# Kernel optimization log

Hardware: AMD Instinct MI355X
Metric: run time of the kernel (lower is better)

## Reference

```python
import jax, jax.numpy as jnp
import numpy as np
import math

L_LAYERS = 2; B = 2; SEQ = 1024; D = 512; N = 16; H = 8; DH = 64; P = 32; KC = 4; DTR = 32

def _silu(x):
    return x * jax.nn.sigmoid(x)

def _rms(x, w, eps=1e-6):
    return x * jax.lax.rsqrt(jnp.mean(x * x, axis=-1, keepdims=True) + eps) * w

def _mamba(x, Win, conv_w, conv_b, Wx, Wdt, bdt, Alog, Dp, Wout):
    # x: [b,l,d]; mamba-ssm reference math with expand=1 (d_inner == d)
    b, l, d = x.shape
    xz = x @ Win                                   # [b,l,2d]
    xc, z = jnp.split(xz, 2, axis=-1)
    xp = jnp.pad(xc, ((0, 0), (KC - 1, 0), (0, 0)))  # causal depthwise conv
    xc = sum(xp[:, k:k + l, :] * conv_w[:, k] for k in range(KC)) + conv_b
    xc = _silu(xc)
    dbl = xc @ Wx                                  # [b,l,dtr+2N]
    dt = dbl[..., :DTR]
    Bc = dbl[..., DTR:DTR + N]                     # [b,l,N]
    Cc = dbl[..., DTR + N:]                        # [b,l,N]
    dt = jax.nn.softplus(dt @ Wdt + bdt)           # [b,l,d]
    A = -jnp.exp(Alog)                             # [d,N]
    dA = jnp.exp(dt[..., None] * A)                # [b,l,d,N]
    dBu = dt[..., None] * Bc[:, :, None, :] * xc[..., None]  # [b,l,d,N]
    def step(h, inp):
        dA_t, dBu_t, C_t = inp
        h = dA_t * h + dBu_t                       # [b,d,N]
        return h, jnp.einsum('bdn,bn->bd', h, C_t)
    h0 = jnp.zeros((b, d, N), x.dtype)
    _, ys = jax.lax.scan(step, h0, (dA.transpose(1, 0, 2, 3), dBu.transpose(1, 0, 2, 3), Cc.transpose(1, 0, 2)))
    y = ys.transpose(1, 0, 2) + Dp * xc
    y = y * _silu(z)
    return y @ Wout

def _enformer_attn(q, k, vv, u, vb, w):
    # q,k,vv: [b,l,h,d]; u,vb: [h,d]; w: [h,d,P]
    b, l, h, d = q.shape
    Pd = w.shape[-1]
    pos = jnp.arange(l)
    dist = pos[None, :] - pos[:, None]             # [l,l]
    pow_rate = jnp.exp(jnp.log((l + 1) / 2.0) / (Pd // 2))
    cw = pow_rate ** jnp.arange(1, Pd // 2 + 1, dtype=jnp.float32)
    ub = (jnp.abs(dist)[:, :, None].astype(jnp.float32) <= cw)
    sb = jnp.sign(dist)[:, :, None].astype(jnp.float32) * ub.astype(jnp.float32)
    basis = jnp.concatenate([ub.astype(jnp.float32), sb], axis=-1)  # [l,l,P]
    scale = 1.0 / math.sqrt(d)
    # qr_term without materializing r[h,l,l,d]: (q@w) then contract with basis
    qw = jnp.einsum('bihd,hdn->bhin', q, w)
    qr = jnp.einsum('bhin,ijn->bhij', qw, basis)
    uk = jnp.einsum('hd,bjhd->bhj', u, k)[:, :, None, :]
    vr = jnp.einsum('hn,ijn->hij', jnp.einsum('hd,hdn->hn', vb, w), basis)
    scores = jnp.einsum('bihd,bjhd->bhij', q, k) * scale + (qr + uk + vr[None]) * scale
    attn = jax.nn.softmax(scores, axis=-1)
    return jnp.einsum('bhij,bjhd->bihd', attn, vv)

def _forward(x, rms_m, W_in, b_in, m_Win, m_conv_w, m_conv_b, m_Wx, m_Wdt, m_bdt, m_Alog, m_D, m_Wout, W_out, b_out, rms_a, Wq, Wk, Wv, u, v, w_rel, Wo, b_o):
    b, l, dm = x.shape
    for i in range(L_LAYERS):
        # --- BidirectionalMamba block (tie_in_proj=True, tie_gate=False) ---
        skip = x
        xn = _rms(x, rms_m[i])
        proj = xn @ W_in[i] + b_in[i]              # [b,l,3*dm]
        xf = proj[..., :dm]
        zf = proj[..., dm:2 * dm]
        zr = proj[..., 2 * dm:]
        yf = _mamba(xf, m_Win[i, 0], m_conv_w[i, 0], m_conv_b[i, 0], m_Wx[i, 0], m_Wdt[i, 0], m_bdt[i, 0], m_Alog[i, 0], m_D[i, 0], m_Wout[i, 0])
        yr = jnp.flip(_mamba(jnp.flip(xf, axis=1), m_Win[i, 1], m_conv_w[i, 1], m_conv_b[i, 1], m_Wx[i, 1], m_Wdt[i, 1], m_bdt[i, 1], m_Alog[i, 1], m_D[i, 1], m_Wout[i, 1]), axis=1)
        y = yf * _silu(zf) + yr * _silu(zr)
        x = y @ W_out[i] + b_out[i] + skip
        # --- Enformer relative-position attention block ---
        skip = x
        xn = _rms(x, rms_a[i])
        q = (xn @ Wq[i]).reshape(b, l, H, DH)
        k = (xn @ Wk[i]).reshape(b, l, H, DH)
        vv = (xn @ Wv[i]).reshape(b, l, H, DH)
        o = _enformer_attn(q, k, vv, u[i], v[i], w_rel[i]).reshape(b, l, H * DH)
        x = skip + o @ Wo[i] + b_o[i]
    return x

def setup_inputs() -> dict:
    key = jax.random.key(0)
    ks = iter(jax.random.split(key, 48))
    def rn(shape, s=0.02):
        return jax.random.normal(next(ks), shape, dtype=jnp.float32) * s
    L = L_LAYERS
    inp = {}
    inp['x'] = jax.random.normal(next(ks), (B, SEQ, D), dtype=jnp.float32)
    inp['rms_m'] = jnp.ones((L, D), jnp.float32)
    inp['W_in'] = rn((L, D, 3 * D)); inp['b_in'] = jnp.zeros((L, 3 * D), jnp.float32)
    inp['m_Win'] = rn((L, 2, D, 2 * D))
    inp['m_conv_w'] = rn((L, 2, D, KC), 0.1); inp['m_conv_b'] = jnp.zeros((L, 2, D), jnp.float32)
    inp['m_Wx'] = rn((L, 2, D, DTR + 2 * N))
    inp['m_Wdt'] = rn((L, 2, DTR, D), 0.1); inp['m_bdt'] = rn((L, 2, D), 0.5)
    inp['m_Alog'] = jnp.tile(jnp.log(jnp.arange(1, N + 1, dtype=jnp.float32)), (L, 2, D, 1))
    inp['m_D'] = jnp.ones((L, 2, D), jnp.float32)
    inp['m_Wout'] = rn((L, 2, D, D))
    inp['W_out'] = rn((L, D, D)); inp['b_out'] = jnp.zeros((L, D), jnp.float32)
    inp['rms_a'] = jnp.ones((L, D), jnp.float32)
    inp['Wq'] = rn((L, D, H * DH)); inp['Wk'] = rn((L, D, H * DH)); inp['Wv'] = rn((L, D, H * DH))
    inp['u'] = rn((L, H, DH), 0.1); inp['v'] = rn((L, H, DH), 0.1)
    inp['w_rel'] = rn((L, H, DH, P), 0.1)
    inp['Wo'] = rn((L, H * DH, D)); inp['b_o'] = jnp.zeros((L, D), jnp.float32)
    return inp

def reference(x, rms_m, W_in, b_in, m_Win, m_conv_w, m_conv_b, m_Wx, m_Wdt, m_bdt, m_Alog, m_D, m_Wout, W_out, b_out, rms_a, Wq, Wk, Wv, u, v, w_rel, Wo, b_o):
    return _forward(x, rms_m, W_in, b_in, m_Win, m_conv_w, m_conv_b, m_Wx, m_Wdt, m_bdt, m_Alog, m_D, m_Wout, W_out, b_out, rms_a, Wq, Wk, Wv, u, v, w_rel, Wo, b_o)
```

## Files before the change

kernel.cpp:

```cpp
#include <hip/hip_runtime.h>

#define LL 2
#define BB 2
#define SEQL 1024
#define DD 512
#define NN 16
#define HH 8
#define DHH 64
#define PPB 32
#define KCC 4
#define DTRR 32

#define GBS 4
#define TC 64
#define NC (SEQL / TC)
#define NR (GBS * DD * NN)

#define AR_L     4325376L
#define OFF_WIN  0L
#define OFF_MWIN 786432L
#define OFF_WT2  1835008L
#define OFF_MWOUT 2490368L
#define OFF_WOUT 3014656L
#define OFF_QKV  3276800L
#define OFF_WO   4063232L

typedef __attribute__((ext_vector_type(8))) short bf16x8;
typedef __attribute__((ext_vector_type(4))) short short4v;
typedef __attribute__((ext_vector_type(4))) float f32x4;

__device__ __forceinline__ float siluf(float x) { return x / (1.f + expf(-x)); }
__device__ __forceinline__ float softplusf(float x) { return x > 20.f ? x : log1pf(expf(x)); }

__device__ __forceinline__ unsigned short f2bf(float x) {
  union { float f; unsigned u; } v; v.f = x;
  unsigned r = v.u + 0x7fff + ((v.u >> 16) & 1);
  return (unsigned short)(r >> 16);
}

__device__ __forceinline__ bf16x8 ld_frag(const unsigned short* p) {
  short4v a = *(const short4v*)(p);
  short4v b = *(const short4v*)(p + 4);
  bf16x8 r;
  r[0]=a[0]; r[1]=a[1]; r[2]=a[2]; r[3]=a[3];
  r[4]=b[0]; r[5]=b[1]; r[6]=b[2]; r[7]=b[3];
  return r;
}

__device__ __forceinline__ bf16x8 pack8(const float* p) {
  bf16x8 r;
  #pragma unroll
  for (int e = 0; e < 8; e++) r[e] = (short)f2bf(p[e]);
  return r;
}

struct TD { const float* src; unsigned short* dst; int ldsrc; int K; int N; int t0; };
struct TDs { TD a[24]; };

__global__ __launch_bounds__(256) void wtrans_all(TDs ds)
{
  int bid = blockIdx.x;
  int mi = 0;
  #pragma unroll 1
  for (int i = 1; i < 24; i++) if (bid >= ds.a[i].t0) mi = i;
  TD d = ds.a[mi];
  int local = bid - d.t0;
  int tilesN = d.N >> 5;
  int tn = local % tilesN, tk = local / tilesN;
  __shared__ float t[32][33];
  int tx = threadIdx.x & 31, ty = threadIdx.x >> 5;
  int n0 = tn * 32, k0 = tk * 32;
  #pragma unroll
  for (int i = 0; i < 4; i++)
    t[ty + 8 * i][tx] = d.src[(long)(k0 + ty + 8 * i) * d.ldsrc + n0 + tx];
  __syncthreads();
  #pragma unroll
  for (int i = 0; i < 4; i++)
    d.dst[(long)(n0 + ty + 8 * i) * d.K + k0 + tx] = f2bf(t[tx][ty + 8 * i]);
}

__global__ __launch_bounds__(256) void weff_kernel(
    const float* __restrict__ Wx, const float* __restrict__ Wdt,
    unsigned short* __restrict__ WTA)
{
  int lg = blockIdx.z;
  int l = lg >> 1, g = lg & 1;
  const float* wx = Wx + (long)(l * 2 + g) * DD * 64;
  const float* wd = Wdt + (long)(l * 2 + g) * DTRR * DD;
  unsigned short* wt = WTA + (long)l * AR_L + OFF_WT2 + (long)g * 327680;
  int n0 = blockIdx.x * 32, k0 = blockIdx.y * 32;
  __shared__ float wx_s[32][33];
  __shared__ float wd_s[32][33];
  int tx = threadIdx.x & 31, ty = threadIdx.x >> 5;
  #pragma unroll
  for (int i = 0; i < 4; i++) {
    wx_s[ty + 8 * i][tx] = wx[(long)(k0 + ty + 8 * i) * 64 + tx];
    wd_s[ty + 8 * i][tx] = wd[(long)(ty + 8 * i) * DD + n0 + tx];
  }
  __syncthreads();
  #pragma unroll
  for (int i = 0; i < 4; i++) {
    int nl = ty + 8 * i;
    float s = 0.f;
    #pragma unroll
    for (int r = 0; r < 32; r++) s = fmaf(wx_s[tx][r], wd_s[r][nl], s);
    wt[(long)(n0 + nl) * DD + k0 + tx] = f2bf(s);
  }
}

__global__ __launch_bounds__(256) void rmsinv_kernel(
    const float* __restrict__ x, float* __restrict__ inv)
{
  int row = blockIdx.x * 4 + (threadIdx.x >> 6);
  int lane = threadIdx.x & 63;
  const float* xr = x + (long)row * DD;
  float4 a = *(const float4*)(xr + lane * 4);
  float4 b = *(const float4*)(xr + 256 + lane * 4);
  float s = a.x*a.x + a.y*a.y + a.z*a.z + a.w*a.w + b.x*b.x + b.y*b.y + b.z*b.z + b.w*b.w;
  for (int o = 32; o; o >>= 1) s += __shfl_down(s, o);
  if (lane == 0) inv[row] = rsqrtf(s / (float)DD + 1e-6f);
}

template<int BM, int BN>
__global__ __launch_bounds__(256) void gemm_bf16_t(
    const float* __restrict__ A, const unsigned short* __restrict__ WT,
    const float* __restrict__ bias, const float* __restrict__ resid,
    const float* __restrict__ invrow, const float* __restrict__ colw,
    float* __restrict__ C,
    int M, int N, int K, int lda, int ldc,
    long aBatch, long wBatch, long biasBatch, long cBatch,
    int aflipL, int act)
{
  constexpr int FM = BM / 32;
  constexpr int FN = BN / 32;
  int g = blockIdx.z;
  A  += (long)g * aBatch;
  WT += (long)g * wBatch;
  C  += (long)g * cBatch;
  if (bias) bias += (long)g * biasBatch;
  const bool flip = (aflipL > 0) && (g == 1);

  __shared__ unsigned short A_lds[BM][72];
  __shared__ unsigned short B_lds[BN][72];
  int tid = threadIdx.x;
  int w = tid >> 6, lane = tid & 63, li = lane & 15, lg = lane >> 4;
  int bm = blockIdx.y * BM, bn = blockIdx.x * BN;
  int wm = (w & 1) * (BM / 2), wn = (w >> 1) * (BN / 2);
  f32x4 acc[FM][FN] = {};

  const int kqA = (tid & 15) * 4, r0A = tid >> 4;
  const int kqB = (tid & 7) * 8,  r0B = tid >> 3;

  for (int k0 = 0; k0 < K; k0 += 64) {
    __syncthreads();
    float4 cw4 = {1.f, 1.f, 1.f, 1.f};
    if (colw) cw4 = *(const float4*)(colw + k0 + kqA);
    #pragma unroll
    for (int i = 0; i < BM / 16; i++) {
      int m = bm + r0A + 16 * i;
      int mm = m;
      if (flip) { int bb = m / aflipL; int t = m - bb * aflipL; mm = bb * aflipL + (aflipL - 1 - t); }
      float4 av = *(const float4*)(A + (long)mm * lda + k0 + kqA);
      float sc = invrow ? invrow[mm] : 1.f;
      short4v ap = { (short)f2bf(av.x * sc * cw4.x), (short)f2bf(av.y * sc * cw4.y),
                     (short)f2bf(av.z * sc * cw4.z), (short)f2bf(av.w * sc * cw4.w) };
      *(short4v*)(&A_lds[r0A + 16 * i][kqA]) = ap;
    }
    #pragma unroll
    for (int i = 0; i < BN / 32; i++) {
      int n = bn + r0B + 32 * i;
      bf16x8 bv = *(const bf16x8*)(WT + (long)n * K + k0 + kqB);
      *(bf16x8*)(&B_lds[r0B + 32 * i][kqB]) = bv;
    }
    __syncthreads();
    #pragma unroll
    for (int ks = 0; ks < 2; ks++) {
      bf16x8 af[FM], bfr[FN];
      #pragma unroll
      for (int fm = 0; fm < FM; fm++)
        af[fm] = *(const bf16x8*)(&A_lds[wm + fm * 16 + li][ks * 32 + lg * 8]);
      #pragma unroll
      for (int fn = 0; fn < FN; fn++)
        bfr[fn] = *(const bf16x8*)(&B_lds[wn + fn * 16 + li][ks * 32 + lg * 8]);
      #pragma unroll
      for (int fm = 0; fm < FM; fm++)
        #pragma unroll
        for (int fn = 0; fn < FN; fn++)
          acc[fm][fn] = __builtin_amdgcn_mfma_f32_16x16x32_bf16(af[fm], bfr[fn], acc[fm][fn], 0, 0, 0);
    }
  }
  #pragma unroll
  for (int fm = 0; fm < FM; fm++) {
    #pragma unroll
    for (int fn = 0; fn < FN; fn++) {
      int n = bn + wn + fn * 16 + li;
      float bv = bias ? bias[n] : 0.f;
      #pragma unroll
      for (int r = 0; r < 4; r++) {
        int m = bm + wm + fm * 16 + 4 * lg + r;
        float v = acc[fm][fn][r] + bv;
        if (act == 1) v = softplusf(v);
        if (resid) v += resid[(long)m * ldc + n];
        C[(long)m * ldc + n] = v;
      }
    }
  }
}

__global__ __launch_bounds__(256) void gemm_dtbc(
    const float* __restrict__ A, const unsigned short* __restrict__ WT2,
    const float* __restrict__ bdt, float* __restrict__ dtv, float* __restrict__ bc,
    int layer)
{
  int g = blockIdx.z;
  A   += (long)g * BB * SEQL * DD;
  WT2 += (long)g * 640 * DD;
  dtv += (long)g * BB * SEQL * DD;
  bc  += (long)g * BB * SEQL * 32;
  bdt += (long)(layer * 2 + g) * DD;

  __shared__ unsigned short A_lds[64][72];
  __shared__ unsigned short B_lds[64][72];
  int tid = threadIdx.x;
  int w = tid >> 6, lane = tid & 63, li = lane & 15, lg = lane >> 4;
  int bm = blockIdx.y * 64, bn = blockIdx.x * 64;
  int wm = (w & 1) * 32, wn = (w >> 1) * 32;
  f32x4 acc[2][2] = {};

  const int kqA = (tid & 15) * 4, r0A = tid >> 4;
  const int kqB = (tid & 7) * 8,  r0B = tid >> 3;

  for (int k0 = 0; k0 < DD; k0 += 64) {
    __syncthreads();
    #pragma unroll
    for (int i = 0; i < 4; i++) {
      int m = bm + r0A + 16 * i;
      float4 av = *(const float4*)(A + (long)m * DD + k0 + kqA);
      short4v ap = { (short)f2bf(av.x), (short)f2bf(av.y), (short)f2bf(av.z), (short)f2bf(av.w) };
      *(short4v*)(&A_lds[r0A + 16 * i][kqA]) = ap;
    }
    #pragma unroll
    for (int i = 0; i < 2; i++) {
      int n = bn + r0B + 32 * i;
      bf16x8 bv = *(const bf16x8*)(WT2 + (long)n * DD + k0 + kqB);
      *(bf16x8*)(&B_lds[r0B + 32 * i][kqB]) = bv;
    }
    __syncthreads();
    #pragma unroll
    for (int ks = 0; ks < 2; ks++) {
      bf16x8 af[2], bfr[2];
      #pragma unroll
      for (int fm = 0; fm < 2; fm++)
        af[fm] = *(const bf16x8*)(&A_lds[wm + fm * 16 + li][ks * 32 + lg * 8]);
      #pragma unroll
      for (int fn = 0; fn < 2; fn++)
        bfr[fn] = *(const bf16x8*)(&B_lds[wn + fn * 16 + li][ks * 32 + lg * 8]);
      #pragma unroll
      for (int fm = 0; fm < 2; fm++)
        #pragma unroll
        for (int fn = 0; fn < 2; fn++)
          acc[fm][fn] = __builtin_amdgcn_mfma_f32_16x16x32_bf16(af[fm], bfr[fn], acc[fm][fn], 0, 0, 0);
    }
  }
  #pragma unroll
  for (int fm = 0; fm < 2; fm++) {
    #pragma unroll
    for (int fn = 0; fn < 2; fn++) {
      int n = bn + wn + fn * 16 + li;
      if (n < 512) {
        float bv = bdt[n];
        #pragma unroll
        for (int r = 0; r < 4; r++) {
          int m = bm + wm + fm * 16 + 4 * lg + r;
          dtv[(long)m * DD + n] = softplusf(acc[fm][fn][r] + bv);
        }
      } else if (n < 544) {
        #pragma unroll
        for (int r = 0; r < 4; r++) {
          int m = bm + wm + fm * 16 + 4 * lg + r;
          bc[(long)m * 32 + (n - 512)] = acc[fm][fn][r];
        }
      }
    }
  }
}

__global__ __launch_bounds__(256) void conv_silu_kernel(
    const float* __restrict__ xz, const float* __restrict__ cw, const float* __restrict__ cb,
    float* __restrict__ xc, int layer)
{
  long idx = (long)blockIdx.x * 256 + threadIdx.x;
  int c = idx % DD;
  long r = idx / DD;
  int t = r % SEQL;
  long gb = r / SEQL;
  int g = (int)(gb / BB);
  const float* w = cw + ((long)(layer * 2 + g) * DD + c) * KCC;
  float acc = cb[(long)(layer * 2 + g) * DD + c];
  const float* xp = xz + (r - t) * 2 * DD + c;
  #pragma unroll
  for (int k = 0; k < KCC; k++) {
    int tt = t - (KCC - 1) + k;
    if (tt >= 0) acc = fmaf(xp[(long)tt * 2 * DD], w[k], acc);
  }
  xc[idx] = siluf(acc);
}

__global__ __launch_bounds__(256) void scan_chunk_kernel(
    const float* __restrict__ dtv, const float* __restrict__ xc,
    const float* __restrict__ bc, const float* __restrict__ Alog,
    float* __restrict__ P, float* __restrict__ Hend, int layer)
{
  int chunk = blockIdx.x, dtile = blockIdx.y, gb = blockIdx.z;
  int g = gb / BB;
  int tid = threadIdx.x;
  int n = tid & 15, dl = tid >> 4;
  int d = dtile * 16 + dl;
  int t0 = chunk * TC;
  __shared__ float dtv_s[TC][16], xc_s[TC][16], B_s[TC][17];
  {
    int c = tid & 15, rr = tid >> 4;
    long base = ((long)gb * SEQL + t0) * DD + dtile * 16;
    long dbase = ((long)gb * SEQL + t0) * 32;
    #pragma unroll
    for (int i = 0; i < 4; i++) {
      int tl = rr + i * 16;
      dtv_s[tl][c] = dtv[base + (long)tl * DD + c];
      xc_s[tl][c]  = xc[base + (long)tl * DD + c];
      B_s[tl][c]   = bc[dbase + (long)tl * 32 + c];
    }
  }
  __syncthreads();
  float a = -expf(Alog[((long)((layer * 2 + g) * DD) + d) * NN + n]);
  float h = 0.f, sdt = 0.f;
  #pragma unroll 4
  for (int t = 0; t < TC; t++) {
    float dt = dtv_s[t][dl];
    float dA = expf(dt * a);
    h = fmaf(dA, h, dt * B_s[t][n] * xc_s[t][dl]);
    sdt += dt;
  }
  int r = (gb * DD + d) * NN + n;
  long o = (long)chunk * NR + r;
  P[o] = expf(a * sdt);
  Hend[o] = h;
}

__global__ __launch_bounds__(256) void scan_combine_kernel(
    const float* __restrict__ P, const float* __restrict__ Hend, float* __restrict__ Hin)
{
  int r = blockIdx.x * 256 + threadIdx.x;
  float h = 0.f;
  #pragma unroll
  for (int c = 0; c < NC; c++) {
    Hin[(long)c * NR + r] = h;
    h = fmaf(P[(long)c * NR + r], h, Hend[(long)c * NR + r]);
  }
}

__global__ __launch_bounds__(256) void scan_apply_kernel(
    const float* __restrict__ dtv, const float* __restrict__ xc, const float* __restrict__ xz,
    const float* __restrict__ bc, const float* __restrict__ Alog, const float* __restrict__ Dp,
    const float* __restrict__ Hin, float* __restrict__ ym, int layer)
{
  int chunk = blockIdx.x, dtile = blockIdx.y, gb = blockIdx.z;
  int g = gb / BB;
  int tid = threadIdx.x;
  int n = tid & 15, dl = tid >> 4;
  int d = dtile * 16 + dl;
  int t0 = chunk * TC;
  __shared__ float dtv_s[TC][16], xc_s[TC][16], B_s[TC][17], C_s[TC][17], y_s[TC][16];
  {
    int c = tid & 15, rr = tid >> 4;
    long base = ((long)gb * SEQL + t0) * DD + dtile * 16;
    long dbase = ((long)gb * SEQL + t0) * 32;
    #pragma unroll
    for (int i = 0; i < 4; i++) {
      int tl = rr + i * 16;
      dtv_s[tl][c] = dtv[base + (long)tl * DD + c];
      xc_s[tl][c]  = xc[base + (long)tl * DD + c];
      B_s[tl][c]   = bc[dbase + (long)tl * 32 + c];
      C_s[tl][c]   = bc[dbase + (long)tl * 32 + 16 + c];
    }
  }
  __syncthreads();
  float a = -expf(Alog[((long)((layer * 2 + g) * DD) + d) * NN + n]);
  int r = (gb * DD + d) * NN + n;
  float h = Hin[(long)chunk * NR + r];
  #pragma unroll 4
  for (int t = 0; t < TC; t++) {
    float dt = dtv_s[t][dl];
    float dA = expf(dt * a);
    h = fmaf(dA, h, dt * B_s[t][n] * xc_s[t][dl]);
    float val = h * C_s[t][n];
    val += __shfl_xor(val, 1);
    val += __shfl_xor(val, 2);
    val += __shfl_xor(val, 4);
    val += __shfl_xor(val, 8);
    if (n == 0) y_s[t][dl] = val;
  }
  __syncthreads();
  {
    int c = tid & 15, rr = tid >> 4;
    long base = ((long)gb * SEQL + t0) * DD + dtile * 16;
    long zbase = ((long)gb * SEQL + t0) * 2 * DD + DD + dtile * 16;
    float Dpc = Dp[(long)(layer * 2 + g) * DD + dtile * 16 + c];
    #pragma unroll
    for (int i = 0; i < 4; i++) {
      int tl = rr + i * 16;
      float z = xz[zbase + (long)tl * 2 * DD + c];
      ym[base + (long)tl * DD + c] = (y_s[tl][c] + Dpc * xc_s[tl][c]) * siluf(z);
    }
  }
}

__global__ __launch_bounds__(256) void combine_kernel(
    const float* __restrict__ yp, const float* __restrict__ proj, float* __restrict__ yc)
{
  long idx = (long)blockIdx.x * 256 + threadIdx.x;
  int d = idx % DD;
  long r = idx / DD;
  int t = r % SEQL;
  long b = r / SEQL;
  float y0 = yp[idx];
  float y1 = yp[(long)BB * SEQL * DD + (b * SEQL + (SEQL - 1 - t)) * (long)DD + d];
  const float* pr = proj + r * 3 * DD;
  float zf = pr[DD + d];
  float zr = pr[2 * DD + d];
  yc[idx] = y0 * siluf(zf) + y1 * siluf(zr);
}

__global__ void tab_kernel(unsigned short* __restrict__ tab)
{
  int idx = blockIdx.x * blockDim.x + threadIdx.x;
  if (idx >= 2047) return;
  int di = idx - 1023;
  int ad = di < 0 ? -di : di;
  float pr = expf(logf((SEQL + 1) * 0.5f) / 16.0f);
  int n0 = 16;
  for (int n = 15; n >= 0; n--) {
    float cw = powf(pr, (float)(n + 1));
    if ((float)ad <= cw) n0 = n;
  }
  tab[idx] = (unsigned short)(di == 0 ? 34 : (di < 0 ? n0 : 17 + n0));
}

__global__ __launch_bounds__(256) void qw_kernel(
    const float* __restrict__ q, const float* __restrict__ w_rel, float* __restrict__ S, int layer)
{
  int itile = blockIdx.x;
  int bh = blockIdx.y;
  int h = bh % HH, b = bh / HH;
  int i0 = itile * 64;
  __shared__ float q_s[64][65];
  __shared__ float w_s[64][33];
  __shared__ float qwn[64][33];
  int tid = threadIdx.x;
  {
    int r = tid >> 2, c4 = (tid & 3) * 16;
    const float* qr = q + ((long)(b * SEQL + i0 + r)) * DD + h * 64 + c4;
    #pragma unroll
    for (int e = 0; e < 4; e++) {
      float4 v = *(const float4*)(qr + e * 4);
      q_s[r][c4 + e * 4 + 0] = v.x; q_s[r][c4 + e * 4 + 1] = v.y;
      q_s[r][c4 + e * 4 + 2] = v.z; q_s[r][c4 + e * 4 + 3] = v.w;
    }
  }
  for (int idx = tid; idx < 64 * 32; idx += 256) {
    int d = idx >> 5, n = idx & 31;
    w_s[d][n] = w_rel[((long)(layer * HH + h) * DHH + d) * PPB + n];
  }
  __syncthreads();
  {
    int i = tid & 63, ngrp = tid >> 6;
    float acc[8] = {};
    #pragma unroll 8
    for (int d = 0; d < 64; d++) {
      float qv = q_s[i][d];
      #pragma unroll
      for (int e = 0; e < 8; e++) acc[e] = fmaf(qv, w_s[d][ngrp * 8 + e], acc[e]);
    }
    #pragma unroll
    for (int e = 0; e < 8; e++) qwn[i][ngrp * 8 + e] = acc[e];
  }
  __syncthreads();
  for (int idx = tid; idx < 64 * 17; idx += 256) {
    int il = idx / 17, m = idx % 17;
    float s1 = 0.f, s2 = 0.f;
    for (int n = m; n < 16; n++) { s1 += qwn[il][n]; s2 += qwn[il][16 + n]; }
    float* Sp = S + ((long)bh * SEQL + i0 + il) * 34;
    Sp[m] = s1;
    Sp[17 + m] = s2;
  }
}

__global__ __launch_bounds__(256) void vw_kernel(
    const float* __restrict__ vparam, const float* __restrict__ w_rel, float* __restrict__ VS, int layer)
{
  __shared__ float vws[HH][PPB];
  int tid = threadIdx.x;
  int h = tid / PPB, n = tid % PPB;
  const float* vp = vparam + (long)(layer * HH + h) * DHH;
  const float* wp = w_rel + ((long)(layer * HH + h) * DHH) * PPB + n;
  float s = 0.f;
  for (int d = 0; d < DHH; d++) s = fmaf(vp[d], wp[d * PPB], s);
  vws[h][n] = s;
  __syncthreads();
  if (tid < HH * 17) {
    int hh = tid / 17, m = tid % 17;
    float s1 = 0.f, s2 = 0.f;
    for (int nn = m; nn < 16; nn++) { s1 += vws[hh][nn]; s2 += vws[hh][16 + nn]; }
    VS[hh * 34 + m] = s1;
    VS[hh * 34 + 17 + m] = s2;
  }
}

__global__ __launch_bounds__(256) void uk_kernel(
    const float* __restrict__ u, const float* __restrict__ k, float* __restrict__ uk, int layer)
{
  int wid = (blockIdx.x * 256 + threadIdx.x) >> 6;
  int lane = threadIdx.x & 63;
  if (wid >= BB * HH * SEQL) return;
  int j = wid % SEQL;
  int bh = wid / SEQL;
  int h = bh % HH;
  int b = bh / HH;
  float vv = u[(long)(layer * HH + h) * DHH + lane] * k[((long)(b * SEQL + j) * HH + h) * DHH + lane];
  for (int o = 32; o; o >>= 1) vv += __shfl_down(vv, o);
  if (lane == 0) uk[(long)bh * SEQL + j] = vv;
}

__global__ __launch_bounds__(256) void attn_mfma_kernel(
    const float* __restrict__ q, const float* __restrict__ k, const float* __restrict__ vv,
    const float* __restrict__ S, const float* __restrict__ VS, const float* __restrict__ uk,
    const unsigned short* __restrict__ tab, float* __restrict__ out)
{
  __shared__ __align__(16) char smem[39680];
  unsigned short* K_lds  = (unsigned short*)(smem);
  unsigned short* VT_lds = (unsigned short*)(smem + 8704);
  unsigned short* PT_lds = (unsigned short*)(smem + 17408);
  float* E               = (float*)(smem + 26112);
  unsigned short* tab_s  = (unsigned short*)(smem + 35328);
  float* uk_s            = (float*)(smem + 39424);
  float* O_lds           = (float*)(smem);

  int itile = blockIdx.x;
  int bh = blockIdx.y;
  int h = bh % HH, b = bh / HH;
  int i0 = itile * 64;
  int tid = threadIdx.x;
  int w = tid >> 6;
  int lane = tid & 63;
  int li = lane & 15, lg = lane >> 4;

  for (int idx = tid; idx < 64 * 17; idx += 256) {
    int il = idx / 17, m = idx % 17;
    long srow = ((long)bh * SEQL + i0 + il) * 34;
    float c0 = S[srow + m]      + VS[h * 34 + m];
    float c1 = S[srow + 17 + m] + VS[h * 34 + 17 + m];
    E[il * 36 + m]      = c0 - c1;
    E[il * 36 + 17 + m] = c0 + c1;
    if (m == 0) E[il * 36 + 34] = c0;
  }
  for (int idx = tid; idx < 2047; idx += 256) tab_s[idx] = tab[idx];

  int iq = i0 + w * 16 + li;
  const float* qrow = q + ((long)(b * SEQL + iq)) * DD + h * 64;
  bf16x8 qf0 = pack8(qrow + 8 * lg);
  bf16x8 qf1 = pack8(qrow + 32 + 8 * lg);

  f32x4 oacc[4] = {};
  float mrun = -1e30f, lrun = 0.f;
  const int ibase = i0 + w * 16 + li;
  unsigned short* PTw = PT_lds + w * 16 * 68;
  const float* Erow = E + (w * 16 + li) * 36;

  for (int j0 = 0; j0 < SEQL; j0 += 64) {
    __syncthreads();
    {
      int jl = tid >> 4;
      int dq = (tid & 15) * 4;
      #pragma unroll
      for (int rr = 0; rr < 4; rr++) {
        int jj = jl + rr * 16;
        long grow = ((long)(b * SEQL + j0 + jj)) * DD + h * 64 + dq;
        float4 kv = *(const float4*)(k + grow);
        short4v kp = { (short)f2bf(kv.x), (short)f2bf(kv.y), (short)f2bf(kv.z), (short)f2bf(kv.w) };
        *(short4v*)(K_lds + jj * 68 + dq) = kp;
        float4 vvv = *(const float4*)(vv + grow);
        VT_lds[(dq + 0) * 68 + jj] = f2bf(vvv.x);
        VT_lds[(dq + 1) * 68 + jj] = f2bf(vvv.y);
        VT_lds[(dq + 2) * 68 + jj] = f2bf(vvv.z);
        VT_lds[(dq + 3) * 68 + jj] = f2bf(vvv.w);
      }
      if (tid < 64) uk_s[tid] = uk[(long)bh * SEQL + j0 + tid];
    }
    __syncthreads();

    f32x4 sf[4];
    #pragma unroll
    for (int jj = 0; jj < 4; jj++) {
      f32x4 c = {};
      c = __builtin_amdgcn_mfma_f32_16x16x32_bf16(
            ld_frag(K_lds + (jj * 16 + li) * 68 + 8 * lg), qf0, c, 0, 0, 0);
      c = __builtin_amdgcn_mfma_f32_16x16x32_bf16(
            ld_frag(K_lds + (jj * 16 + li) * 68 + 32 + 8 * lg), qf1, c, 0, 0, 0);
      sf[jj] = c;
    }

    float sv[4][4];
    float tmax = -1e30f;
    #pragma unroll
    for (int jj = 0; jj < 4; jj++) {
      #pragma unroll
      for (int r = 0; r < 4; r++) {
        int jloc = jj * 16 + 4 * lg + r;
        int di = (j0 + jloc) - ibase;
        int id = tab_s[1023 + di];
        float val = (sf[jj][r] + Erow[id] + uk_s[jloc]) * 0.125f;
        sv[jj][r] = val;
        tmax = fmaxf(tmax, val);
      }
    }
    tmax = fmaxf(tmax, __shfl_xor(tmax, 16));
    tmax = fmaxf(tmax, __shfl_xor(tmax, 32));
    float mnew = fmaxf(mrun, tmax);
    float fsc = __expf(mrun - mnew);
    mrun = mnew;
    lrun *= fsc;
    #pragma unroll
    for (int df = 0; df < 4; df++) oacc[df] *= fsc;

    float psum = 0.f;
    #pragma unroll
    for (int jj = 0; jj < 4; jj++) {
      short4v pk;
      #pragma unroll
      for (int r = 0; r < 4; r++) {
        float p = __expf(sv[jj][r] - mnew);
        psum += p;
        pk[r] = (short)f2bf(p);
      }
      *(short4v*)(PTw + li * 68 + jj * 16 + 4 * lg) = pk;
    }
    psum += __shfl_xor(psum, 16);
    psum += __shfl_xor(psum, 32);
    lrun += psum;

    asm volatile("s_waitcnt lgkmcnt(0)" ::: "memory");

    bf16x8 pf0 = ld_frag(PTw + li * 68 + 8 * lg);
    bf16x8 pf1 = ld_frag(PTw + li * 68 + 32 + 8 * lg);
    #pragma unroll
    for (int df = 0; df < 4; df++) {
      f32x4 c = oacc[df];
      c = __builtin_amdgcn_mfma_f32_16x16x32_bf16(
            ld_frag(VT_lds + (df * 16 + li) * 68 + 8 * lg), pf0, c, 0, 0, 0);
      c = __builtin_amdgcn_mfma_f32_16x16x32_bf16(
            ld_frag(VT_lds + (df * 16 + li) * 68 + 32 + 8 * lg), pf1, c, 0, 0, 0);
      oacc[df] = c;
    }
  }

  __syncthreads();
  float inv = 1.f / lrun;
  #pragma unroll
  for (int df = 0; df < 4; df++) {
    f32x4 o = oacc[df] * inv;
    *(f32x4*)(O_lds + (w * 16 + li) * 68 + df * 16 + 4 * lg) = o;
  }
  __syncthreads();
  {
    int il = tid >> 2, c0 = (tid & 3) * 16;
    long orow = ((long)(b * SEQL + i0 + il)) * DD + h * 64 + c0;
    #pragma unroll
    for (int c4 = 0; c4 < 4; c4++) {
      f32x4 o = *(const f32x4*)(O_lds + il * 68 + c0 + c4 * 4);
      *(f32x4*)(out + orow + c4 * 4) = o;
    }
  }
}

extern "C" void kernel_launch(void* const* d_in, const int* in_sizes, int n_in,
                              void* d_out, int out_size, void* d_ws, size_t ws_size,
                              hipStream_t stream) {
  const float* x_in     = (const float*)d_in[0];
  const float* rms_m    = (const float*)d_in[1];
  const float* W_in     = (const float*)d_in[2];
  const float* b_in     = (const float*)d_in[3];
  const float* m_Win    = (const float*)d_in[4];
  const float* m_conv_w = (const float*)d_in[5];
  const float* m_conv_b = (const float*)d_in[6];
  const float* m_Wx     = (const float*)d_in[7];
  const float* m_Wdt    = (const float*)d_in[8];
  const float* m_bdt    = (const float*)d_in[9];
  const float* m_Alog   = (const float*)d_in[10];
  const float* m_Dp     = (const float*)d_in[11];
  const float* m_Wout   = (const float*)d_in[12];
  const float* W_out    = (const float*)d_in[13];
  const float* b_out    = (const float*)d_in[14];
  const float* rms_a    = (const float*)d_in[15];
  const float* Wq       = (const float*)d_in[16];
  const float* Wk       = (const float*)d_in[17];
  const float* Wv       = (const float*)d_in[18];
  const float* u_p      = (const float*)d_in[19];
  const float* v_p      = (const float*)d_in[20];
  const float* w_rel    = (const float*)d_in[21];
  const float* Wo       = (const float*)d_in[22];
  const float* b_o      = (const float*)d_in[23];
  float* out = (float*)d_out;

  float* ws = (float*)d_ws;
  const long U = (long)BB * SEQL * DD;
  float* xA    = ws;
  float* xB    = ws + 1 * U;
  float* xn    = ws + 2 * U;
  float* proj  = ws + 3 * U;
  float* xz    = ws + 6 * U;
  float* xc    = ws + 10 * U;
  float* dtv   = ws + 12 * U;
  float* ym    = ws + 14 * U;
  float* ycomb = ws + 16 * U;
  float* smallb= ws + 17 * U;
  float* bcbuf = smallb;
  float* ukbuf = smallb + 262144;
  float* Sbuf  = smallb + 278528;
  float* VSbuf = smallb + 835584;
  unsigned short* tabg = (unsigned short*)(smallb + 835856);
  float* invm  = smallb + 836880;
  float* inva  = smallb + 838928;
  unsigned short* WTA = (unsigned short*)(ws + 18 * U);
  float* yp = xz;
  float* qb = proj;
  float* kb = proj + U;
  float* vb = proj + 2 * U;
  float* attnout = ym;
  float* Pbuf = xn;
  float* Hend = xn + (long)NC * NR;
  float* Hin  = ycomb;

  const int M = BB * SEQL;

  tab_kernel<<<8, 256, 0, stream>>>(tabg);

  TDs td;
  int cum = 0, idx = 0;
  auto add = [&](const float* s, unsigned short* dst, int ldsrc, int K, int N) {
    td.a[idx].src = s; td.a[idx].dst = dst; td.a[idx].ldsrc = ldsrc;
    td.a[idx].K = K; td.a[idx].N = N; td.a[idx].t0 = cum;
    cum += (N / 32) * (K / 32); idx++;
  };
  for (int l = 0; l < LL; l++) {
    unsigned short* base = WTA + (long)l * AR_L;
    add(W_in   + (long)l * DD * 3 * DD,        base + OFF_WIN,            3 * DD, DD, 3 * DD);
    add(m_Win  + (long)(l * 2 + 0) * DD * 2 * DD, base + OFF_MWIN,          2 * DD, DD, 2 * DD);
    add(m_Win  + (long)(l * 2 + 1) * DD * 2 * DD, base + OFF_MWIN + 524288, 2 * DD, DD, 2 * DD);
    add(m_Wout + (long)(l * 2 + 0) * DD * DD,  base + OFF_MWOUT,          DD, DD, DD);
    add(m_Wout + (long)(l * 2 + 1) * DD * DD,  base + OFF_MWOUT + 262144, DD, DD, DD);
    add(W_out  + (long)l * DD * DD,            base + OFF_WOUT,           DD, DD, DD);
    add(Wq     + (long)l * DD * DD,            base + OFF_QKV,            DD, DD, DD);
    add(Wk     + (long)l * DD * DD,            base + OFF_QKV + 262144,   DD, DD, DD);
    add(Wv     + (long)l * DD * DD,            base + OFF_QKV + 524288,   DD, DD, DD);
    add(Wo     + (long)l * DD * DD,            base + OFF_WO,             DD, DD, DD);
    add(m_Wx   + (long)(l * 2 + 0) * DD * 64 + 32, base + OFF_WT2 + 262144,          64, DD, 32);
    add(m_Wx   + (long)(l * 2 + 1) * DD * 64 + 32, base + OFF_WT2 + 327680 + 262144, 64, DD, 32);
  }
  wtrans_all<<<cum, 256, 0, stream>>>(td);
  weff_kernel<<<dim3(16, 16, 2 * LL), 256, 0, stream>>>(m_Wx, m_Wdt, WTA);

  for (int layer = 0; layer < LL; layer++) {
    const float* cur = (layer == 0) ? x_in : xA;
    unsigned short* base = WTA + (long)layer * AR_L;
    rmsinv_kernel<<<M / 4, 256, 0, stream>>>(cur, invm);
    gemm_bf16_t<64, 64><<<dim3(24, 32, 1), 256, 0, stream>>>(cur, base + OFF_WIN,
        b_in + layer * 3 * DD, nullptr, invm, rms_m + layer * DD, proj,
        M, 3 * DD, DD, DD, 3 * DD, 0, 0, 0, 0, 0, 0);
    gemm_bf16_t<64, 64><<<dim3(16, 32, 2), 256, 0, stream>>>(proj, base + OFF_MWIN,
        nullptr, nullptr, nullptr, nullptr, xz, M, 2 * DD, DD, 3 * DD, 2 * DD,
        0, 524288, 0, (long)BB * SEQL * 2 * DD, SEQL, 0);
    conv_silu_kernel<<<(2 * BB * SEQL * DD) / 256, 256, 0, stream>>>(xz, m_conv_w, m_conv_b, xc, layer);
    gemm_dtbc<<<dim3(9, 32, 2), 256, 0, stream>>>(xc, base + OFF_WT2, m_bdt, dtv, bcbuf, layer);
    scan_chunk_kernel<<<dim3(NC, DD / 16, GBS), 256, 0, stream>>>(
        dtv, xc, bcbuf, m_Alog, Pbuf, Hend, layer);
    scan_combine_kernel<<<NR / 256, 256, 0, stream>>>(Pbuf, Hend, Hin);
    scan_apply_kernel<<<dim3(NC, DD / 16, GBS), 256, 0, stream>>>(
        dtv, xc, xz, bcbuf, m_Alog, m_Dp, Hin, ym, layer);
    gemm_bf16_t<64, 64><<<dim3(8, 32, 2), 256, 0, stream>>>(ym, base + OFF_MWOUT,
        nullptr, nullptr, nullptr, nullptr, yp, M, DD, DD, DD, DD,
        U, 262144, 0, U, 0, 0);
    combine_kernel<<<(int)(U / 256), 256, 0, stream>>>(yp, proj, ycomb);
    gemm_bf16_t<64, 64><<<dim3(8, 32, 1), 256, 0, stream>>>(ycomb, base + OFF_WOUT,
        b_out + layer * DD, cur, nullptr, nullptr, xB, M, DD, DD, DD, DD, 0, 0, 0, 0, 0, 0);

    rmsinv_kernel<<<M / 4, 256, 0, stream>>>(xB, inva);
    gemm_bf16_t<64, 64><<<dim3(8, 32, 3), 256, 0, stream>>>(xB, base + OFF_QKV,
        nullptr, nullptr, inva, rms_a + layer * DD, qb, M, DD, DD, DD, DD,
        0, 262144, 0, U, 0, 0);
    qw_kernel<<<dim3(16, 16), 256, 0, stream>>>(qb, w_rel, Sbuf, layer);
    vw_kernel<<<1, 256, 0, stream>>>(v_p, w_rel, VSbuf, layer);
    uk_kernel<<<(BB * HH * SEQL) / 4, 256, 0, stream>>>(u_p, kb, ukbuf, layer);
    attn_mfma_kernel<<<dim3(SEQL / 64, BB * HH), 256, 0, stream>>>(
        qb, kb, vb, Sbuf, VSbuf, ukbuf, tabg, attnout);

    float* outp = (layer == LL - 1) ? out : xA;
    gemm_bf16_t<64, 64><<<dim3(8, 32, 1), 256, 0, stream>>>(attnout, base + OFF_WO,
        b_o + layer * DD, xB, nullptr, nullptr, outp, M, DD, DD, DD, DD, 0, 0, 0, 0, 0, 0);
  }
}
```

Baseline: 657.2 us.

## Split attention over key halves with a combine pass, use fast exp

The attention kernel now splits the key range into two halves across a third grid dimension. Each block writes unnormalized partial outputs plus running max and sum, and a new combine kernel merges them with log-sum-exp rescaling. This doubles the block count (256 to 512) so more of the GPU is occupied. The change also swaps expf for __expf in silu, softplus and the scan kernels, and hoists the v·w_rel precompute out of the layer loop into one launch. In exchange it adds partial-buffer traffic, an extra kernel launch per layer, and slightly reduced exp accuracy.

```diff
diff --git a/kernel.cpp b/kernel.cpp
--- a/kernel.cpp
+++ b/kernel.cpp
@@ -15,6 +15,7 @@
 #define TC 64
 #define NC (SEQL / TC)
 #define NR (GBS * DD * NN)
+#define BHN (BB * HH * SEQL)
 
 #define AR_L     4325376L
 #define OFF_WIN  0L
@@ -29,8 +30,8 @@
 typedef __attribute__((ext_vector_type(4))) short short4v;
 typedef __attribute__((ext_vector_type(4))) float f32x4;
 
-__device__ __forceinline__ float siluf(float x) { return x / (1.f + expf(-x)); }
-__device__ __forceinline__ float softplusf(float x) { return x > 20.f ? x : log1pf(expf(x)); }
+__device__ __forceinline__ float siluf(float x) { return x / (1.f + __expf(-x)); }
+__device__ __forceinline__ float softplusf(float x) { return x > 20.f ? x : log1pf(__expf(x)); }
 
 __device__ __forceinline__ unsigned short f2bf(float x) {
   union { float f; unsigned u; } v; v.f = x;
@@ -331,18 +332,18 @@
     }
   }
   __syncthreads();
-  float a = -expf(Alog[((long)((layer * 2 + g) * DD) + d) * NN + n]);
+  float a = -__expf(Alog[((long)((layer * 2 + g) * DD) + d) * NN + n]);
   float h = 0.f, sdt = 0.f;
   #pragma unroll 4
   for (int t = 0; t < TC; t++) {
     float dt = dtv_s[t][dl];
-    float dA = expf(dt * a);
+    float dA = __expf(dt * a);
     h = fmaf(dA, h, dt * B_s[t][n] * xc_s[t][dl]);
     sdt += dt;
   }
   int r = (gb * DD + d) * NN + n;
   long o = (long)chunk * NR + r;
-  P[o] = expf(a * sdt);
+  P[o] = __expf(a * sdt);
   Hend[o] = h;
 }
 
@@ -384,13 +385,13 @@
     }
   }
   __syncthreads();
-  float a = -expf(Alog[((long)((layer * 2 + g) * DD) + d) * NN + n]);
+  float a = -__expf(Alog[((long)((layer * 2 + g) * DD) + d) * NN + n]);
   int r = (gb * DD + d) * NN + n;
   float h = Hin[(long)chunk * NR + r];
   #pragma unroll 4
   for (int t = 0; t < TC; t++) {
     float dt = dtv_s[t][dl];
-    float dA = expf(dt * a);
+    float dA = __expf(dt * a);
     h = fmaf(dA, h, dt * B_s[t][n] * xc_s[t][dl]);
     float val = h * C_s[t][n];
     val += __shfl_xor(val, 1);
@@ -495,8 +496,9 @@
 }
 
 __global__ __launch_bounds__(256) void vw_kernel(
-    const float* __restrict__ vparam, const float* __restrict__ w_rel, float* __restrict__ VS, int layer)
-{
+    const float* __restrict__ vparam, const float* __restrict__ w_rel, float* __restrict__ VS)
+{
+  int layer = blockIdx.x;
   __shared__ float vws[HH][PPB];
   int tid = threadIdx.x;
   int h = tid / PPB, n = tid % PPB;
@@ -510,8 +512,8 @@
     int hh = tid / 17, m = tid % 17;
     float s1 = 0.f, s2 = 0.f;
     for (int nn = m; nn < 16; nn++) { s1 += vws[hh][nn]; s2 += vws[hh][16 + nn]; }
-    VS[hh * 34 + m] = s1;
-    VS[hh * 34 + 17 + m] = s2;
+    VS[layer * 272 + hh * 34 + m] = s1;
+    VS[layer * 272 + hh * 34 + 17 + m] = s2;
   }
 }
 
@@ -533,7 +535,8 @@
 __global__ __launch_bounds__(256) void attn_mfma_kernel(
     const float* __restrict__ q, const float* __restrict__ k, const float* __restrict__ vv,
     const float* __restrict__ S, const float* __restrict__ VS, const float* __restrict__ uk,
-    const unsigned short* __restrict__ tab, float* __restrict__ out)
+    const unsigned short* __restrict__ tab,
+    float* __restrict__ opart, float* __restrict__ mbuf, float* __restrict__ lbuf)
 {
   __shared__ __align__(16) char smem[39680];
   unsigned short* K_lds  = (unsigned short*)(smem);
@@ -546,6 +549,7 @@
 
   int itile = blockIdx.x;
   int bh = blockIdx.y;
+  int split = blockIdx.z;
   int h = bh % HH, b = bh / HH;
   int i0 = itile * 64;
   int tid = threadIdx.x;
@@ -575,7 +579,9 @@
   unsigned short* PTw = PT_lds + w * 16 * 68;
   const float* Erow = E + (w * 16 + li) * 36;
 
-  for (int j0 = 0; j0 < SEQL; j0 += 64) {
+  const int jbase = split * (SEQL / 2);
+  for (int jt = 0; jt < SEQL / 2; jt += 64) {
+    int j0 = jbase + jt;
     __syncthreads();
     {
       int jl = tid >> 4;
@@ -663,22 +669,41 @@
   }
 
   __syncthreads();
-  float inv = 1.f / lrun;
-  #pragma unroll
-  for (int df = 0; df < 4; df++) {
-    f32x4 o = oacc[df] * inv;
-    *(f32x4*)(O_lds + (w * 16 + li) * 68 + df * 16 + 4 * lg) = o;
-  }
+  if (lg == 0) {
+    long row = (long)split * BHN + (long)bh * SEQL + (i0 + w * 16 + li);
+    mbuf[row] = mrun;
+    lbuf[row] = lrun;
+  }
+  #pragma unroll
+  for (int df = 0; df < 4; df++)
+    *(f32x4*)(O_lds + (w * 16 + li) * 68 + df * 16 + 4 * lg) = oacc[df];
   __syncthreads();
   {
     int il = tid >> 2, c0 = (tid & 3) * 16;
-    long orow = ((long)(b * SEQL + i0 + il)) * DD + h * 64 + c0;
+    long orow = ((long)split * BHN + (long)bh * SEQL + i0 + il) * 64 + c0;
     #pragma unroll
     for (int c4 = 0; c4 < 4; c4++) {
       f32x4 o = *(const f32x4*)(O_lds + il * 68 + c0 + c4 * 4);
-      *(f32x4*)(out + orow + c4 * 4) = o;
-    }
-  }
+      *(f32x4*)(opart + orow + c4 * 4) = o;
+    }
+  }
+}
+
+__global__ __launch_bounds__(256) void attn_combine_kernel(
+    const float* __restrict__ opart, const float* __restrict__ mbuf,
+    const float* __restrict__ lbuf, float* __restrict__ out)
+{
+  int idx = blockIdx.x * 256 + threadIdx.x;
+  int row = idx >> 6, d = idx & 63;
+  int bh = row >> 10, i = row & 1023;
+  int b = bh >> 3, h = bh & 7;
+  float m0 = mbuf[row], m1 = mbuf[BHN + row];
+  float l0 = lbuf[row], l1 = lbuf[BHN + row];
+  float m = fmaxf(m0, m1);
+  float e0 = __expf(m0 - m), e1 = __expf(m1 - m);
+  float inv = 1.f / (l0 * e0 + l1 * e1);
+  float o = (opart[(long)row * 64 + d] * e0 + opart[((long)BHN + row) * 64 + d] * e1) * inv;
+  out[((long)(b * SEQL + i)) * DD + h * 64 + d] = o;
 }
 
 extern "C" void kernel_launch(void* const* d_in, const int* in_sizes, int n_in,
@@ -726,9 +751,9 @@
   float* ukbuf = smallb + 262144;
   float* Sbuf  = smallb + 278528;
   float* VSbuf = smallb + 835584;
-  unsigned short* tabg = (unsigned short*)(smallb + 835856);
-  float* invm  = smallb + 836880;
-  float* inva  = smallb + 838928;
+  unsigned short* tabg = (unsigned short*)(smallb + 836880);
+  float* invm  = smallb + 838928;
+  float* inva  = smallb + 840976;
   unsigned short* WTA = (unsigned short*)(ws + 18 * U);
   float* yp = xz;
   float* qb = proj;
@@ -738,6 +763,9 @@
   float* Pbuf = xn;
   float* Hend = xn + (long)NC * NR;
   float* Hin  = ycomb;
+  float* opart = xc;
+  float* mbuf  = dtv;
+  float* lbuf  = dtv + 2 * BHN;
 
   const int M = BB * SEQL;
 
@@ -767,6 +795,7 @@
   }
   wtrans_all<<<cum, 256, 0, stream>>>(td);
   weff_kernel<<<dim3(16, 16, 2 * LL), 256, 0, stream>>>(m_Wx, m_Wdt, WTA);
+  vw_kernel<<<LL, 256, 0, stream>>>(v_p, w_rel, VSbuf);
 
   for (int layer = 0; layer < LL; layer++) {
     const float* cur = (layer == 0) ? x_in : xA;
@@ -797,10 +826,10 @@
         nullptr, nullptr, inva, rms_a + layer * DD, qb, M, DD, DD, DD, DD,
         0, 262144, 0, U, 0, 0);
     qw_kernel<<<dim3(16, 16), 256, 0, stream>>>(qb, w_rel, Sbuf, layer);
-    vw_kernel<<<1, 256, 0, stream>>>(v_p, w_rel, VSbuf, layer);
     uk_kernel<<<(BB * HH * SEQL) / 4, 256, 0, stream>>>(u_p, kb, ukbuf, layer);
-    attn_mfma_kernel<<<dim3(SEQL / 64, BB * HH), 256, 0, stream>>>(
-        qb, kb, vb, Sbuf, VSbuf, ukbuf, tabg, attnout);
+    attn_mfma_kernel<<<dim3(SEQL / 64, BB * HH, 2), 256, 0, stream>>>(
+        qb, kb, vb, Sbuf, VSbuf + layer * 272, ukbuf, tabg, opart, mbuf, lbuf);
+    attn_combine_kernel<<<(BHN * 64) / 256, 256, 0, stream>>>(opart, mbuf, lbuf, attnout);
 
     float* outp = (layer == LL - 1) ? out : xA;
     gemm_bf16_t<64, 64><<<dim3(8, 32, 1), 256, 0, stream>>>(attnout, base + OFF_WO,
```

After: 614.5 us. 1.07x faster.
